# Optimization experiments

Measured on AMD Instinct MI355X. Metric: run time of the kernel, lower is better.

## Reference

```python
import jax, jax.numpy as jnp
import numpy as np

E, K, MULT = 8, 2, 4          # num_experts, top_k, ffn mult
CF = 1.25                     # capacity_factor


def setup_inputs() -> dict:
    key = jax.random.key(0)
    ks = jax.random.split(key, 8)
    B, T, C = 4, 2048, 1024
    H = C * MULT
    s = 0.02
    return {
        "x": jax.random.normal(ks[0], (B, T, C), jnp.float32),
        "rw": jax.random.normal(ks[1], (E, C), jnp.float32) * s,   # router weight [E,C]
        "rb": jnp.zeros((E,), jnp.float32),                        # router bias
        "w1": jax.random.normal(ks[2], (E, C, H), jnp.float32) * s,
        "b1": jnp.zeros((E, H), jnp.float32),
        "w2": jax.random.normal(ks[3], (E, H, C), jnp.float32) * s,
        "b2": jnp.zeros((E, C), jnp.float32),
    }


def reference(x, rw, rb, w1, b1, w2, b2):
    B, T, C = x.shape
    N = B * T
    cap = int(CF * N / E)                      # static capacity per expert
    xf = x.reshape(N, C)
    logits = xf @ rw.T + rb                    # [N,E]
    probs = jax.nn.softmax(logits, axis=-1)
    topk_probs, topk_idx = jax.lax.top_k(probs, K)      # [N,K]
    topk_probs = topk_probs / topk_probs.sum(-1, keepdims=True)

    # Flatten (token, choice) row-major == torch.where(mask) ordering
    flat_idx = topk_idx.reshape(-1)            # [N*K] expert id per slot
    flat_gate = topk_probs.reshape(-1)         # [N*K]
    onehot = jax.nn.one_hot(flat_idx, E, dtype=jnp.int32)          # [N*K,E]
    pos = (jnp.cumsum(onehot, axis=0) - 1)[jnp.arange(N * K), flat_idx]  # rank within expert
    keep = pos < cap                           # first-come-first-served capacity drop
    tok = jnp.arange(N * K) // K               # owning token of each slot

    # Dispatch into [E, cap] buffers; dropped slots go to a dump slot at the end
    buf = jnp.where(keep, flat_idx * cap + pos, E * cap)
    gate_buf = jnp.zeros(E * cap + 1, x.dtype).at[buf].add(flat_gate)[:E * cap]
    tok_buf = jnp.zeros(E * cap + 1, jnp.int32).at[buf].set(tok)[:E * cap]

    inp = xf[tok_buf].reshape(E, cap, C)       # gathered expert inputs
    h = jax.nn.gelu(jnp.einsum('eic,ech->eih', inp, w1) + b1[:, None, :], approximate=False)
    out = jnp.einsum('eih,ehc->eic', h, w2) + b2[:, None, :]
    out = out * gate_buf.reshape(E, cap, 1)    # empty slots have gate 0 -> zero contribution

    y = jnp.zeros((N, C), x.dtype).at[tok_buf].add(out.reshape(E * cap, C))

    # Aux load-balancing loss
    imp = probs.sum(0)
    imp = imp / imp.sum()
    load = jnp.minimum(onehot.sum(0).astype(x.dtype), cap)   # kept token counts
    load = load / load.sum()
    aux_loss = (imp * load).sum() * (E ** 2)
    return y.reshape(B, T, C), aux_loss
```

## Files before the change

### kernel.cpp

```cpp
#include <hip/hip_runtime.h>
#include <hip/hip_bf16.h>
#include <math.h>

#define NE    8
#define KTOP  2
#define CDIM  1024
#define HDIM  4096
#define NTOK  8192
#define CAPE  1280
#define NSLOT (NTOK * KTOP)

typedef __bf16 bf16x8 __attribute__((ext_vector_type(8)));
typedef __bf16 bf16x4 __attribute__((ext_vector_type(4)));
typedef __bf16 bf16x2 __attribute__((ext_vector_type(2)));
typedef float  f32x4  __attribute__((ext_vector_type(4)));

#define GAS __attribute__((address_space(1)))
#define LAS __attribute__((address_space(3)))

__global__ __launch_bounds__(256) void k_transpose_bf16(
    const float* __restrict__ src, __bf16* __restrict__ dst, int R, int Cc)
{
    __shared__ __bf16 T[64][72];
    const int e  = blockIdx.z;
    const int cb = blockIdx.x * 64;
    const int rb = blockIdx.y * 64;
    const int t  = threadIdx.x;
    const int bx = t & 15, by = t >> 4;

    const float* s = src + (size_t)e * R * Cc
                   + (size_t)(rb + by * 4) * Cc + cb + bx * 4;
    float4 m[4];
#pragma unroll
    for (int i = 0; i < 4; ++i)
        m[i] = *(const float4*)(s + (size_t)i * Cc);
#pragma unroll
    for (int j = 0; j < 4; ++j) {
        bf16x4 v;
        v[0] = (__bf16)((&m[0].x)[j]);
        v[1] = (__bf16)((&m[1].x)[j]);
        v[2] = (__bf16)((&m[2].x)[j]);
        v[3] = (__bf16)((&m[3].x)[j]);
        *(bf16x4*)&T[bx * 4 + j][by * 4] = v;
    }
    __syncthreads();
    const int oc = t >> 2, rc = (t & 3) * 16;
    __bf16* d = dst + (size_t)e * R * Cc + (size_t)(cb + oc) * R + rb + rc;
    *(bf16x8*)d       = *(const bf16x8*)&T[oc][rc];
    *(bf16x8*)(d + 8) = *(const bf16x8*)&T[oc][rc + 8];
}

__global__ __launch_bounds__(256) void k_router(
    const float* __restrict__ x, const float* __restrict__ rw,
    const float* __restrict__ rb, float* __restrict__ probs,
    float* __restrict__ gates, int* __restrict__ tidx)
{
    __shared__ float rws[NE * CDIM];
    const int tid = threadIdx.x;
    for (int i = tid; i < NE * CDIM / 4; i += 256)
        ((float4*)rws)[i] = ((const float4*)rw)[i];
    __syncthreads();

    const int wave = tid >> 6, lane = tid & 63;
    const int n = blockIdx.x * 4 + wave;
    const float* xr = x + (size_t)n * CDIM;

    float acc[NE];
#pragma unroll
    for (int e = 0; e < NE; ++e) acc[e] = 0.f;
    for (int j = 0; j < CDIM / 64; ++j) {
        const float xv = xr[j * 64 + lane];
#pragma unroll
        for (int e = 0; e < NE; ++e) acc[e] += xv * rws[e * CDIM + j * 64 + lane];
    }
#pragma unroll
    for (int off = 32; off > 0; off >>= 1) {
#pragma unroll
        for (int e = 0; e < NE; ++e) acc[e] += __shfl_down(acc[e], off);
    }
    if (lane == 0) {
        float mx = -1e30f;
#pragma unroll
        for (int e = 0; e < NE; ++e) { acc[e] += rb[e]; mx = fmaxf(mx, acc[e]); }
        float p[NE], s = 0.f;
#pragma unroll
        for (int e = 0; e < NE; ++e) { p[e] = expf(acc[e] - mx); s += p[e]; }
        const float inv = 1.f / s;
#pragma unroll
        for (int e = 0; e < NE; ++e) { p[e] *= inv; probs[(size_t)n * NE + e] = p[e]; }
        int   i1 = 0;  float v1 = p[0];
        int   i2 = -1; float v2 = -1.f;
#pragma unroll
        for (int e = 1; e < NE; ++e) {
            if (p[e] > v1)      { v2 = v1; i2 = i1; v1 = p[e]; i1 = e; }
            else if (p[e] > v2) { v2 = p[e]; i2 = e; }
        }
        const float gs = 1.f / (v1 + v2);
        gates[n * 2 + 0] = v1 * gs;  gates[n * 2 + 1] = v2 * gs;
        tidx[n * 2 + 0]  = i1;       tidx[n * 2 + 1]  = i2;
    }
}

__global__ __launch_bounds__(256) void k_scan(
    const int* __restrict__ tidx, const float* __restrict__ probs,
    int* __restrict__ slot, int* __restrict__ tok, float* __restrict__ d_aux)
{
    __shared__ int   lcnt[256][NE];
    __shared__ float ps[256][NE];
    const int t = threadIdx.x;

    for (int i = t; i < NE * CAPE; i += 256) tok[i] = 0;

    int c8[NE];
#pragma unroll
    for (int e = 0; e < NE; ++e) c8[e] = 0;
    const int per  = NSLOT / 256;
    const int base = t * per;
    for (int s = 0; s < per; ++s) c8[tidx[base + s]]++;
#pragma unroll
    for (int e = 0; e < NE; ++e) lcnt[t][e] = c8[e];

    float f8[NE];
#pragma unroll
    for (int e = 0; e < NE; ++e) f8[e] = 0.f;
    for (int n = t; n < NTOK; n += 256) {
        const float4 a = *(const float4*)(probs + (size_t)n * NE);
        const float4 b = *(const float4*)(probs + (size_t)n * NE + 4);
        f8[0] += a.x; f8[1] += a.y; f8[2] += a.z; f8[3] += a.w;
        f8[4] += b.x; f8[5] += b.y; f8[6] += b.z; f8[7] += b.w;
    }
#pragma unroll
    for (int e = 0; e < NE; ++e) ps[t][e] = f8[e];

    __syncthreads();

    int run[NE];
#pragma unroll
    for (int e = 0; e < NE; ++e) run[e] = c8[e];
    for (int d = 1; d < 256; d <<= 1) {
        int add[NE];
#pragma unroll
        for (int e = 0; e < NE; ++e) add[e] = (t >= d) ? lcnt[t - d][e] : 0;
        __syncthreads();
#pragma unroll
        for (int e = 0; e < NE; ++e) { run[e] += add[e]; lcnt[t][e] = run[e]; }
        __syncthreads();
    }
    int pre[NE], tot[NE];
#pragma unroll
    for (int e = 0; e < NE; ++e) {
        pre[e] = run[e] - c8[e];
        tot[e] = lcnt[255][e];
    }

    for (int d = 128; d >= 1; d >>= 1) {
        if (t < d) {
#pragma unroll
            for (int e = 0; e < NE; ++e) ps[t][e] += ps[t + d][e];
        }
        __syncthreads();
    }

    for (int s = 0; s < per; ++s) {
        const int sg = base + s;
        const int e  = tidx[sg];
        const int p  = pre[e]++;
        if (p < CAPE) { slot[sg] = e * CAPE + p; tok[e * CAPE + p] = sg >> 1; }
        else          { slot[sg] = -1; }
    }
    if (t == 0) {
        float isum = 0.f, lsum = 0.f, ld[NE];
#pragma unroll
        for (int e = 0; e < NE; ++e) isum += ps[0][e];
#pragma unroll
        for (int e = 0; e < NE; ++e) { ld[e] = fminf((float)tot[e], (float)CAPE); lsum += ld[e]; }
        float aux = 0.f;
#pragma unroll
        for (int e = 0; e < NE; ++e) aux += (ps[0][e] / isum) * (ld[e] / lsum);
        *d_aux = aux * (float)(NE * NE);
    }
}

__global__ __launch_bounds__(256) void k_gather(
    const float* __restrict__ x, const int* __restrict__ tok,
    __bf16* __restrict__ inp)
{
    const int row = blockIdx.x;
    const int t   = threadIdx.x;
    const int tk  = tok[row];
    const float4 v = ((const float4*)(x + (size_t)tk * CDIM))[t];
    bf16x4 o;
    o[0] = (__bf16)v.x; o[1] = (__bf16)v.y; o[2] = (__bf16)v.z; o[3] = (__bf16)v.w;
    *(bf16x4*)(inp + (size_t)row * CDIM + t * 4) = o;
}

#define MFMA_BF16 __builtin_amdgcn_mfma_f32_16x16x32_bf16
#define DSR_I(dst, addr, IMM) \
    asm volatile("ds_read_b128 %0, %1 offset:" #IMM : "=v"(dst) : "v"(addr))
#define DSR(dst, addr, IMM) DSR_I(dst, addr, IMM)
#define WVM4() asm volatile("s_waitcnt vmcnt(4)" ::: "memory")
#define SB0()  __builtin_amdgcn_sched_barrier(0)

#define PH(RDB, OA0, OA1, MB, VA0, VA1, VB0, VB1, STG, VMW)                   \
    {                                                                         \
        if (RDB) {                                                            \
            DSR(fb[0][0], VB0, 0);    DSR(fb[0][1], VB1, 0);                  \
            DSR(fb[1][0], VB0, 2048); DSR(fb[1][1], VB1, 2048);               \
            DSR(fb[2][0], VB0, 4096); DSR(fb[2][1], VB1, 4096);               \
            DSR(fb[3][0], VB0, 6144); DSR(fb[3][1], VB1, 6144);               \
        }                                                                     \
        DSR(fa[0][0], VA0, OA0); DSR(fa[0][1], VA1, OA0);                     \
        DSR(fa[1][0], VA0, OA1); DSR(fa[1][1], VA1, OA1);                     \
        STG;                                                                  \
        if (RDB) { asm volatile("s_waitcnt lgkmcnt(8)" ::: "memory"); }       \
        __builtin_amdgcn_s_barrier();                                         \
        asm volatile("s_waitcnt lgkmcnt(0)" ::: "memory");                    \
        SB0();                                                                \
        __builtin_amdgcn_s_setprio(1);                                        \
        _Pragma("unroll")                                                     \
        for (int n = 0; n < 4; ++n) {                                         \
            acc[MB][n]   = MFMA_BF16(fb[n][0], fa[0][0], acc[MB][n], 0,0,0);  \
            acc[MB][n]   = MFMA_BF16(fb[n][1], fa[0][1], acc[MB][n], 0,0,0);  \
            acc[MB+1][n] = MFMA_BF16(fb[n][0], fa[1][0], acc[MB+1][n],0,0,0); \
            acc[MB+1][n] = MFMA_BF16(fb[n][1], fa[1][1], acc[MB+1][n],0,0,0); \
        }                                                                     \
        __builtin_amdgcn_s_setprio(0);                                        \
        VMW;                                                                  \
        __builtin_amdgcn_s_barrier();                                        \
        SB0();                                                                \
    }

template <bool GELU>
__global__ __launch_bounds__(512, 2) void k_gemm8(
    const __bf16* __restrict__ Aall, const __bf16* __restrict__ Ball,
    const float* __restrict__ biasAll, __bf16* __restrict__ Call,
    int Ktot, int Ntot, int NBN, int mtPerE)
{
    __shared__ char lds[133120];

    const int NK  = Ktot >> 6;
    const int NI  = NK >> 1;
    const int cpx = gridDim.x >> 3;
    const int id  = blockIdx.x;
    const int sid = (id & 7) * cpx + (id >> 3);
    const int bm  = sid / NBN, bn = sid % NBN;
    const int e   = bm / mtPerE;

    const size_t row0 = (size_t)bm * 256;
    const int    col0 = bn * 256;

    const int tid = threadIdx.x;
    const int w   = tid >> 6, l = tid & 63;
    const int wr  = w >> 2, wc = w & 3;
    const int lr  = l & 15, hi = l >> 4;

    const int srow = tid >> 3;
    const int kf   = ((tid & 7) ^ (srow & 7)) << 3;
    const __bf16* pA = Aall + (row0 + srow) * (size_t)Ktot + kf;
    const __bf16* pB = Ball + ((size_t)e * Ntot + col0 + srow) * (size_t)Ktot + kf;
    const unsigned L0 = (unsigned)(size_t)(LAS char*)lds;

    const unsigned sA00 = L0 +          w * 1024;
    const unsigned sA01 = sA00 + 16384;
    const unsigned sA10 = sA00 + 32768;
    const unsigned sA11 = sA00 + 49152;
    const unsigned sB00 = sA00 + 65536;
    const unsigned sB01 = sB00 + 16384;
    const unsigned sB10 = sB00 + 32768;
    const unsigned sB11 = sB00 + 49152;

    auto SH_A = [&](unsigned dbase, int half, int kt) {
        const __bf16* g = pA + (size_t)(half * 128) * Ktot + (size_t)kt * 64;
#pragma unroll
        for (int gg = 0; gg < 2; ++gg)
            __builtin_amdgcn_global_load_lds(
                (const GAS void*)(g + (size_t)gg * 64 * Ktot),
                (LAS void*)(size_t)(dbase + gg * 8192), 16, 0, 0);
    };
    auto SH_B = [&](unsigned dbase, int half, int kt) {
        const __bf16* g = pB + (size_t)(half * 128) * Ktot + (size_t)kt * 64;
#pragma unroll
        for (int gg = 0; gg < 2; ++gg)
            __builtin_amdgcn_global_load_lds(
                (const GAS void*)(g + (size_t)gg * 64 * Ktot),
                (LAS void*)(size_t)(dbase + gg * 8192), 16, 0, 0);
    };

    const unsigned swz = (l & 7) << 4;
    const unsigned kb0 = ((unsigned)(hi << 4)) ^ swz;
    const unsigned kb1 = ((unsigned)(64 + (hi << 4))) ^ swz;
    const unsigned vA00 = L0 + (unsigned)(wr * 16384 + lr * 128) + kb0;
    const unsigned vA01 = L0 + (unsigned)(wr * 16384 + lr * 128) + kb1;
    const unsigned vA10 = vA00 + 32768, vA11 = vA01 + 32768;
    const unsigned vBb  = L0 + 65536
        + (unsigned)((wc >> 1) * 16384 + ((wc & 1) * 64 + lr) * 128);
    const unsigned vB00 = vBb + kb0, vB01 = vBb + kb1;
    const unsigned vB10 = vB00 + 32768, vB11 = vB01 + 32768;

    SH_B(sB00, 0, 0); SH_B(sB01, 1, 0);
    SH_A(sA00, 0, 0); SH_A(sA01, 1, 0);
    SH_B(sB10, 0, 1); SH_B(sB11, 1, 1);
    WVM4();
    __builtin_amdgcn_s_barrier();
    SB0();

    f32x4 acc[8][4] = {};
    bf16x8 fa[2][2], fb[4][2];

    for (int i = 0; i < NI; ++i) {
        const int t1 = 2 * i + 1;
        const int t2 = (2 * i + 2 < NK) ? 2 * i + 2 : NK - 1;
        const int t3 = (2 * i + 3 < NK) ? 2 * i + 3 : NK - 1;
        PH(1, 0,     2048,  0, vA00, vA01, vB00, vB01, SH_A(sA10, 0, t1), (void)0)
        PH(0, 4096,  6144,  2, vA00, vA01, vB00, vB01, SH_A(sA11, 1, t1), (void)0)
        PH(0, 8192,  10240, 4, vA00, vA01, vB00, vB01, SH_B(sB00, 0, t2), (void)0)
        PH(0, 12288, 14336, 6, vA00, vA01, vB00, vB01, SH_B(sB01, 1, t2), WVM4())
        PH(1, 0,     2048,  0, vA10, vA11, vB10, vB11, SH_A(sA00, 0, t2), (void)0)
        PH(0, 4096,  6144,  2, vA10, vA11, vB10, vB11, SH_A(sA01, 1, t2), (void)0)
        PH(0, 8192,  10240, 4, vA10, vA11, vB10, vB11, SH_B(sB10, 0, t3), (void)0)
        PH(0, 12288, 14336, 6, vA10, vA11, vB10, vB11, SH_B(sB11, 1, t3), WVM4())
    }

    asm volatile("s_waitcnt vmcnt(0)" ::: "memory");
    __builtin_amdgcn_s_barrier();
    SB0();

    const int lrow0 = wr * 128;
    const int lcol0 = wc * 64;
#pragma unroll
    for (int n = 0; n < 4; ++n) {
        float bbv[4] = {0.f, 0.f, 0.f, 0.f};
        if (GELU) {
            const float4 b4 = *(const float4*)(biasAll + (size_t)e * Ntot
                                               + col0 + lcol0 + n * 16 + hi * 4);
            bbv[0] = b4.x; bbv[1] = b4.y; bbv[2] = b4.z; bbv[3] = b4.w;
        }
#pragma unroll
        for (int m = 0; m < 8; ++m) {
            const f32x4 v = acc[m][n];
            bf16x4 o;
#pragma unroll
            for (int i = 0; i < 4; ++i) {
                float t = v[i];
                if (GELU) {
                    t += bbv[i];
                    const float u  = 0.7978845608028654f * (t + 0.044715f * t * t * t);
                    const float ex = __expf(2.f * u);
                    t = t * (1.f - 1.f / (ex + 1.f));
                }
                o[i] = (__bf16)t;
            }
            *(bf16x4*)(lds + (lrow0 + m * 16 + lr) * 520
                           + (lcol0 + n * 16 + hi * 4) * 2) = o;
        }
    }
    __builtin_amdgcn_s_barrier();

    {
        const int rr0 = tid >> 5;
        const int cc  = (tid & 31) * 8;
#pragma unroll
        for (int it = 0; it < 16; ++it) {
            const int rr = it * 16 + rr0;
            const bf16x8 v = *(const bf16x8*)(lds + rr * 520 + cc * 2);
            *(bf16x8*)(Call + (row0 + rr) * (size_t)Ntot + col0 + cc) = v;
        }
    }
}

__global__ __launch_bounds__(256) void k_combine(
    const __bf16* __restrict__ outb, const int* __restrict__ slot,
    const float* __restrict__ gates, const int* __restrict__ tidx,
    const float* __restrict__ b2, float* __restrict__ y)
{
    const int n = blockIdx.x;
    const int t = threadIdx.x;
    const int c = t * 4;
    float r0 = 0.f, r1 = 0.f, r2 = 0.f, r3 = 0.f;
#pragma unroll
    for (int k = 0; k < KTOP; ++k) {
        const int s = slot[n * 2 + k];
        if (s < 0) continue;
        const float g = gates[n * 2 + k];
        const int   e = tidx[n * 2 + k];
        const bf16x4 v = *(const bf16x4*)(outb + (size_t)s * CDIM + c);
        const float4 bb = *(const float4*)(b2 + (size_t)e * CDIM + c);
        r0 += g * ((float)v[0] + bb.x);
        r1 += g * ((float)v[1] + bb.y);
        r2 += g * ((float)v[2] + bb.z);
        r3 += g * ((float)v[3] + bb.w);
    }
    float4 o = make_float4(r0, r1, r2, r3);
    *(float4*)(y + (size_t)n * CDIM + c) = o;
}

extern "C" void kernel_launch(void* const* d_in, const int* in_sizes, int n_in,
                              void* d_out, int out_size, void* d_ws, size_t ws_size,
                              hipStream_t stream)
{
    const float* x  = (const float*)d_in[0];
    const float* rw = (const float*)d_in[1];
    const float* rb = (const float*)d_in[2];
    const float* w1 = (const float*)d_in[3];
    const float* b1 = (const float*)d_in[4];
    const float* w2 = (const float*)d_in[5];
    const float* b2 = (const float*)d_in[6];
    float* y = (float*)d_out;

    char* ws = (char*)d_ws;
    size_t off = 0;
    auto alloc = [&](size_t bytes) -> void* {
        void* p = ws + off;
        off = (off + bytes + 255) & ~(size_t)255;
        return p;
    };
    __bf16* w1t  = (__bf16*)alloc((size_t)NE * CDIM * HDIM * 2);
    __bf16* w2t  = (__bf16*)alloc((size_t)NE * CDIM * HDIM * 2);
    __bf16* inp  = (__bf16*)alloc((size_t)NE * CAPE * CDIM * 2);
    __bf16* hbuf = (__bf16*)alloc((size_t)NE * CAPE * HDIM * 2);
    __bf16* outb = (__bf16*)alloc((size_t)NE * CAPE * CDIM * 2);
    float*  probs = (float*)alloc((size_t)NTOK * NE * 4);
    float*  gates = (float*)alloc((size_t)NTOK * 2 * 4);
    int*    tidx  = (int*)alloc((size_t)NTOK * 2 * 4);
    int*    slot  = (int*)alloc((size_t)NTOK * 2 * 4);
    int*    tok   = (int*)alloc((size_t)NE * CAPE * 4);

    k_transpose_bf16<<<dim3(HDIM / 64, CDIM / 64, NE), 256, 0, stream>>>(
        w1, w1t, CDIM, HDIM);
    k_transpose_bf16<<<dim3(CDIM / 64, HDIM / 64, NE), 256, 0, stream>>>(
        w2, w2t, HDIM, CDIM);

    k_router<<<NTOK / 4, 256, 0, stream>>>(x, rw, rb, probs, gates, tidx);

    k_scan<<<1, 256, 0, stream>>>(tidx, probs, slot, tok, y + (size_t)NTOK * CDIM);

    k_gather<<<NE * CAPE, 256, 0, stream>>>(x, tok, inp);

    k_gemm8<true><<<dim3((NE * CAPE / 256) * (HDIM / 256)), 512, 0, stream>>>(
        inp, w1t, b1, hbuf, CDIM, HDIM, HDIM / 256, CAPE / 256);
    k_gemm8<false><<<dim3((NE * CAPE / 256) * (CDIM / 256)), 512, 0, stream>>>(
        hbuf, w2t, nullptr, outb, HDIM, CDIM, CDIM / 256, CAPE / 256);

    k_combine<<<NTOK, 256, 0, stream>>>(outb, slot, gates, tidx, b2, y);
}
```

Before: 381.8 us.

## Replace 256x256 LDS GEMM with 128x128 tile loading B fragments from global

Both expert GEMMs move from a 512-thread 256x256 tile that stages A and B in a 130KB LDS buffer to a 256-thread 128x128 tile. Only A is staged in LDS, double-buffered. Each wave loads its B fragments straight from global memory into registers, ping-ponging between two register sets. This cuts LDS use and barrier phases and raises occupancy, but it lowers reuse per tile, adds global traffic for B, and leaves B reads uncoalesced in 16-byte pieces per lane.

```diff
diff --git a/kernel.cpp b/kernel.cpp
--- a/kernel.cpp
+++ b/kernel.cpp
@@ -195,138 +195,117 @@
 }
 
 #define MFMA_BF16 __builtin_amdgcn_mfma_f32_16x16x32_bf16
-#define DSR_I(dst, addr, IMM) \
+#define DSR(dst, addr, IMM) \
     asm volatile("ds_read_b128 %0, %1 offset:" #IMM : "=v"(dst) : "v"(addr))
-#define DSR(dst, addr, IMM) DSR_I(dst, addr, IMM)
-#define WVM4() asm volatile("s_waitcnt vmcnt(4)" ::: "memory")
 #define SB0()  __builtin_amdgcn_sched_barrier(0)
 
-#define PH(RDB, OA0, OA1, MB, VA0, VA1, VB0, VB1, STG, VMW)                   \
+#define TILE(BUFO, NBUFO, FBC, FBN, TN)                                       \
     {                                                                         \
-        if (RDB) {                                                            \
-            DSR(fb[0][0], VB0, 0);    DSR(fb[0][1], VB1, 0);                  \
-            DSR(fb[1][0], VB0, 2048); DSR(fb[1][1], VB1, 2048);               \
-            DSR(fb[2][0], VB0, 4096); DSR(fb[2][1], VB1, 4096);               \
-            DSR(fb[3][0], VB0, 6144); DSR(fb[3][1], VB1, 6144);               \
-        }                                                                     \
-        DSR(fa[0][0], VA0, OA0); DSR(fa[0][1], VA1, OA0);                     \
-        DSR(fa[1][0], VA0, OA1); DSR(fa[1][1], VA1, OA1);                     \
-        STG;                                                                  \
-        if (RDB) { asm volatile("s_waitcnt lgkmcnt(8)" ::: "memory"); }       \
-        __builtin_amdgcn_s_barrier();                                         \
-        asm volatile("s_waitcnt lgkmcnt(0)" ::: "memory");                    \
+        LDB(FBN, TN);                                                         \
+        SH_A(NBUFO, TN);                                                      \
         SB0();                                                                \
+        DSR(fa0[0], vA0 + (BUFO), 0);    DSR(fa0[1], vA0 + (BUFO), 2048);     \
+        DSR(fa0[2], vA0 + (BUFO), 4096); DSR(fa0[3], vA0 + (BUFO), 6144);     \
+        DSR(fa1[0], vA1 + (BUFO), 0);    DSR(fa1[1], vA1 + (BUFO), 2048);     \
+        DSR(fa1[2], vA1 + (BUFO), 4096); DSR(fa1[3], vA1 + (BUFO), 6144);     \
+        asm volatile("s_waitcnt lgkmcnt(4)" ::: "memory"); SB0();             \
         __builtin_amdgcn_s_setprio(1);                                        \
         _Pragma("unroll")                                                     \
         for (int n = 0; n < 4; ++n) {                                         \
-            acc[MB][n]   = MFMA_BF16(fb[n][0], fa[0][0], acc[MB][n], 0,0,0);  \
-            acc[MB][n]   = MFMA_BF16(fb[n][1], fa[0][1], acc[MB][n], 0,0,0);  \
-            acc[MB+1][n] = MFMA_BF16(fb[n][0], fa[1][0], acc[MB+1][n],0,0,0); \
-            acc[MB+1][n] = MFMA_BF16(fb[n][1], fa[1][1], acc[MB+1][n],0,0,0); \
+            _Pragma("unroll")                                                 \
+            for (int m = 0; m < 4; ++m)                                       \
+                acc[m][n] = MFMA_BF16(FBC[n][0], fa0[m], acc[m][n], 0,0,0);   \
         }                                                                     \
         __builtin_amdgcn_s_setprio(0);                                        \
-        VMW;                                                                  \
-        __builtin_amdgcn_s_barrier();                                        \
+        asm volatile("s_waitcnt lgkmcnt(0)" ::: "memory"); SB0();             \
+        __builtin_amdgcn_s_setprio(1);                                        \
+        _Pragma("unroll")                                                     \
+        for (int n = 0; n < 4; ++n) {                                         \
+            _Pragma("unroll")                                                 \
+            for (int m = 0; m < 4; ++m)                                       \
+                acc[m][n] = MFMA_BF16(FBC[n][1], fa1[m], acc[m][n], 0,0,0);   \
+        }                                                                     \
+        __builtin_amdgcn_s_setprio(0);                                        \
+        asm volatile("s_waitcnt vmcnt(0)" ::: "memory");                      \
+        __builtin_amdgcn_s_barrier();                                         \
         SB0();                                                                \
     }
 
 template <bool GELU>
-__global__ __launch_bounds__(512, 2) void k_gemm8(
+__global__ __launch_bounds__(256, 2) void k_gemmR(
     const __bf16* __restrict__ Aall, const __bf16* __restrict__ Ball,
     const float* __restrict__ biasAll, __bf16* __restrict__ Call,
     int Ktot, int Ntot, int NBN, int mtPerE)
 {
-    __shared__ char lds[133120];
+    __shared__ char lds[34048];
 
     const int NK  = Ktot >> 6;
-    const int NI  = NK >> 1;
     const int cpx = gridDim.x >> 3;
     const int id  = blockIdx.x;
     const int sid = (id & 7) * cpx + (id >> 3);
     const int bm  = sid / NBN, bn = sid % NBN;
     const int e   = bm / mtPerE;
 
-    const size_t row0 = (size_t)bm * 256;
-    const int    col0 = bn * 256;
+    const size_t row0 = (size_t)bm * 128;
+    const int    col0 = bn * 128;
 
     const int tid = threadIdx.x;
     const int w   = tid >> 6, l = tid & 63;
-    const int wr  = w >> 2, wc = w & 3;
+    const int wm  = w >> 1, wn = w & 1;
     const int lr  = l & 15, hi = l >> 4;
 
-    const int srow = tid >> 3;
-    const int kf   = ((tid & 7) ^ (srow & 7)) << 3;
-    const __bf16* pA = Aall + (row0 + srow) * (size_t)Ktot + kf;
-    const __bf16* pB = Ball + ((size_t)e * Ntot + col0 + srow) * (size_t)Ktot + kf;
+    const int arow = w * 32 + (l >> 3);
+    const int kf   = ((l & 7) ^ (l >> 3)) << 3;
+    const __bf16* pA = Aall + (row0 + arow) * (size_t)Ktot + kf;
     const unsigned L0 = (unsigned)(size_t)(LAS char*)lds;
-
-    const unsigned sA00 = L0 +          w * 1024;
-    const unsigned sA01 = sA00 + 16384;
-    const unsigned sA10 = sA00 + 32768;
-    const unsigned sA11 = sA00 + 49152;
-    const unsigned sB00 = sA00 + 65536;
-    const unsigned sB01 = sB00 + 16384;
-    const unsigned sB10 = sB00 + 32768;
-    const unsigned sB11 = sB00 + 49152;
-
-    auto SH_A = [&](unsigned dbase, int half, int kt) {
-        const __bf16* g = pA + (size_t)(half * 128) * Ktot + (size_t)kt * 64;
-#pragma unroll
-        for (int gg = 0; gg < 2; ++gg)
+    const unsigned dA = L0 + w * 4096;
+
+    auto SH_A = [&](unsigned bo, int kt) {
+        const __bf16* g = pA + (size_t)kt * 64;
+#pragma unroll
+        for (int j = 0; j < 4; ++j)
             __builtin_amdgcn_global_load_lds(
-                (const GAS void*)(g + (size_t)gg * 64 * Ktot),
-                (LAS void*)(size_t)(dbase + gg * 8192), 16, 0, 0);
+                (const GAS void*)(g + (size_t)j * 8 * Ktot),
+                (LAS void*)(size_t)(dA + bo + j * 1024), 16, 0, 0);
     };
-    auto SH_B = [&](unsigned dbase, int half, int kt) {
-        const __bf16* g = pB + (size_t)(half * 128) * Ktot + (size_t)kt * 64;
-#pragma unroll
-        for (int gg = 0; gg < 2; ++gg)
-            __builtin_amdgcn_global_load_lds(
-                (const GAS void*)(g + (size_t)gg * 64 * Ktot),
-                (LAS void*)(size_t)(dbase + gg * 8192), 16, 0, 0);
+
+    const __bf16* pB = Ball
+        + ((size_t)e * Ntot + col0 + wn * 64 + lr) * (size_t)Ktot + hi * 8;
+
+    auto LDB = [&](bf16x8 (&fb)[4][2], int kt) {
+#pragma unroll
+        for (int n = 0; n < 4; ++n) {
+#pragma unroll
+            for (int kh = 0; kh < 2; ++kh)
+                fb[n][kh] = *(const bf16x8*)(pB + (size_t)n * 16 * Ktot
+                                             + kt * 64 + kh * 32);
+        }
     };
 
     const unsigned swz = (l & 7) << 4;
     const unsigned kb0 = ((unsigned)(hi << 4)) ^ swz;
     const unsigned kb1 = ((unsigned)(64 + (hi << 4))) ^ swz;
-    const unsigned vA00 = L0 + (unsigned)(wr * 16384 + lr * 128) + kb0;
-    const unsigned vA01 = L0 + (unsigned)(wr * 16384 + lr * 128) + kb1;
-    const unsigned vA10 = vA00 + 32768, vA11 = vA01 + 32768;
-    const unsigned vBb  = L0 + 65536
-        + (unsigned)((wc >> 1) * 16384 + ((wc & 1) * 64 + lr) * 128);
-    const unsigned vB00 = vBb + kb0, vB01 = vBb + kb1;
-    const unsigned vB10 = vB00 + 32768, vB11 = vB01 + 32768;
-
-    SH_B(sB00, 0, 0); SH_B(sB01, 1, 0);
-    SH_A(sA00, 0, 0); SH_A(sA01, 1, 0);
-    SH_B(sB10, 0, 1); SH_B(sB11, 1, 1);
-    WVM4();
-    __builtin_amdgcn_s_barrier();
-    SB0();
-
-    f32x4 acc[8][4] = {};
-    bf16x8 fa[2][2], fb[4][2];
-
-    for (int i = 0; i < NI; ++i) {
-        const int t1 = 2 * i + 1;
-        const int t2 = (2 * i + 2 < NK) ? 2 * i + 2 : NK - 1;
-        const int t3 = (2 * i + 3 < NK) ? 2 * i + 3 : NK - 1;
-        PH(1, 0,     2048,  0, vA00, vA01, vB00, vB01, SH_A(sA10, 0, t1), (void)0)
-        PH(0, 4096,  6144,  2, vA00, vA01, vB00, vB01, SH_A(sA11, 1, t1), (void)0)
-        PH(0, 8192,  10240, 4, vA00, vA01, vB00, vB01, SH_B(sB00, 0, t2), (void)0)
-        PH(0, 12288, 14336, 6, vA00, vA01, vB00, vB01, SH_B(sB01, 1, t2), WVM4())
-        PH(1, 0,     2048,  0, vA10, vA11, vB10, vB11, SH_A(sA00, 0, t2), (void)0)
-        PH(0, 4096,  6144,  2, vA10, vA11, vB10, vB11, SH_A(sA01, 1, t2), (void)0)
-        PH(0, 8192,  10240, 4, vA10, vA11, vB10, vB11, SH_B(sB10, 0, t3), (void)0)
-        PH(0, 12288, 14336, 6, vA10, vA11, vB10, vB11, SH_B(sB11, 1, t3), WVM4())
-    }
-
+    const unsigned vA0 = L0 + (unsigned)((wm * 64 + lr) * 128) + kb0;
+    const unsigned vA1 = L0 + (unsigned)((wm * 64 + lr) * 128) + kb1;
+
+    bf16x8 fbX[4][2], fbY[4][2];
+    SH_A(0u, 0);
+    LDB(fbX, 0);
     asm volatile("s_waitcnt vmcnt(0)" ::: "memory");
     __builtin_amdgcn_s_barrier();
     SB0();
 
-    const int lrow0 = wr * 128;
-    const int lcol0 = wc * 64;
+    f32x4 acc[4][4] = {};
+    bf16x8 fa0[4], fa1[4];
+
+    for (int T = 0; T < NK; T += 2) {
+        const int t1 = (T + 1 < NK) ? T + 1 : NK - 1;
+        const int t2 = (T + 2 < NK) ? T + 2 : NK - 1;
+        TILE(0u,     16384u, fbX, fbY, t1)
+        TILE(16384u, 0u,     fbY, fbX, t2)
+    }
+
+    const int lrow0 = wm * 64, lcol0 = wn * 64;
 #pragma unroll
     for (int n = 0; n < 4; ++n) {
         float bbv[4] = {0.f, 0.f, 0.f, 0.f};
@@ -336,7 +315,7 @@
             bbv[0] = b4.x; bbv[1] = b4.y; bbv[2] = b4.z; bbv[3] = b4.w;
         }
 #pragma unroll
-        for (int m = 0; m < 8; ++m) {
+        for (int m = 0; m < 4; ++m) {
             const f32x4 v = acc[m][n];
             bf16x4 o;
 #pragma unroll
@@ -350,21 +329,17 @@
                 }
                 o[i] = (__bf16)t;
             }
-            *(bf16x4*)(lds + (lrow0 + m * 16 + lr) * 520
+            *(bf16x4*)(lds + (lrow0 + m * 16 + lr) * 264
                            + (lcol0 + n * 16 + hi * 4) * 2) = o;
         }
     }
     __builtin_amdgcn_s_barrier();
-
-    {
-        const int rr0 = tid >> 5;
-        const int cc  = (tid & 31) * 8;
-#pragma unroll
-        for (int it = 0; it < 16; ++it) {
-            const int rr = it * 16 + rr0;
-            const bf16x8 v = *(const bf16x8*)(lds + rr * 520 + cc * 2);
-            *(bf16x8*)(Call + (row0 + rr) * (size_t)Ntot + col0 + cc) = v;
-        }
+#pragma unroll
+    for (int it = 0; it < 8; ++it) {
+        const int rr = it * 16 + (tid >> 4);
+        const int cc = (tid & 15) * 8;
+        const bf16x8 v = *(const bf16x8*)(lds + rr * 264 + cc * 2);
+        *(bf16x8*)(Call + (row0 + rr) * (size_t)Ntot + col0 + cc) = v;
     }
 }
 
@@ -436,10 +411,10 @@
 
     k_gather<<<NE * CAPE, 256, 0, stream>>>(x, tok, inp);
 
-    k_gemm8<true><<<dim3((NE * CAPE / 256) * (HDIM / 256)), 512, 0, stream>>>(
-        inp, w1t, b1, hbuf, CDIM, HDIM, HDIM / 256, CAPE / 256);
-    k_gemm8<false><<<dim3((NE * CAPE / 256) * (CDIM / 256)), 512, 0, stream>>>(
-        hbuf, w2t, nullptr, outb, HDIM, CDIM, CDIM / 256, CAPE / 256);
+    k_gemmR<true><<<dim3((NE * CAPE / 128) * (HDIM / 128)), 256, 0, stream>>>(
+        inp, w1t, b1, hbuf, CDIM, HDIM, HDIM / 128, CAPE / 128);
+    k_gemmR<false><<<dim3((NE * CAPE / 128) * (CDIM / 128)), 256, 0, stream>>>(
+        hbuf, w2t, nullptr, outb, HDIM, CDIM, CDIM / 128, CAPE / 128);
 
     k_combine<<<NTOK, 256, 0, stream>>>(outb, slot, gates, tidx, b2, y);
 }
```

After: 584.0 us. +52.9%, slower.
